# Optimization experiments

Measured on AMD Instinct MI355X. Metric: run time of the kernel, lower is better.

Reference implementation:

```python
import jax, jax.numpy as jnp
import numpy as np

LOW_DIM = 1024
PARAM_DIMS = [(1024, 768), (768,), (768, 256), (256,)]
BLOCK_DIMS = [int(np.prod(d)) for d in PARAM_DIMS]
TOTAL_DIM = int(sum(BLOCK_DIMS))          # 984064
LL = 1 << int(np.ceil(np.log2(TOTAL_DIM)))  # 1048576 = 2^20
BATCH = 32


def fwht(x):
    """Unnormalized fast Walsh-Hadamard transform over the last axis.

    x: [B, L], L a power of two. Butterfly stage order does not change the
    result (H_L = H_2^{\\otimes n}), so this matches the torch chunk/cat loop.
    """
    B, L = x.shape
    h = L // 2
    while h >= 1:
        x = x.reshape(B, -1, 2, h)
        a, b = x[:, :, 0, :], x[:, :, 1, :]
        x = jnp.stack([a + b, a - b], axis=2)
        h //= 2
    return x.reshape(B, L)


def setup_inputs() -> dict:
    key = jax.random.key(0)
    kz, kb, kg = jax.random.split(key, 3)
    z = jax.random.normal(kz, (BATCH, LOW_DIM), dtype=jnp.float32)
    # BB: random signs in {-1, +1}, as in make_fastfood_vars
    BB = jnp.where(jax.random.uniform(kb, (LL,)) < 0.5, -1.0, 1.0).astype(jnp.float32)
    GG = jax.random.normal(kg, (LL,), dtype=jnp.float32)
    Pi = jnp.asarray(np.random.default_rng(0).permutation(LL), dtype=jnp.int32)
    divisor = jnp.sqrt(LL * jnp.sum(GG ** 2)).astype(jnp.float32)
    return {"z": z, "BB": BB, "GG": GG, "divisor": divisor, "Pi": Pi}


def reference(z, BB, GG, divisor, Pi):
    # pad z from low_dim to LL
    dd = jnp.pad(z, ((0, 0), (0, LL - z.shape[1])))      # [B, LL]
    m = fwht(dd * BB[None, :])                           # H (B x)
    m = m[:, Pi] * GG[None, :]                           # G Pi H B x
    m = fwht(m)                                          # H G Pi H B x
    scale = divisor * np.float32(np.sqrt(float(TOTAL_DIM) / LL))
    delta = m[:, :TOTAL_DIM] / scale                     # [B, total_dim]
    outs = []
    off = 0
    for bd, pd in zip(BLOCK_DIMS, PARAM_DIMS):
        outs.append(delta[:, off:off + bd].reshape(-1, *pd))
        off += bd
    return tuple(outs)
```

## Files before the change

kernel.cpp:

```cpp
#include <hip/hip_runtime.h>
#include <math.h>


#define TS 17
#define TOTAL_DIM 984064
#define OUT_B0 786432
#define OUT_B1 787200
#define OUT_B2 983808
#define OFF1 25165824L
#define OFF2 25190400L
#define OFF3 31481856L

template<int CTRL>
__device__ __forceinline__ float pdpp(float x) {
    return __int_as_float(__builtin_amdgcn_update_dpp(
        0, __float_as_int(x), CTRL, 0xF, 0xF, true));
}
template<int OFS>
__device__ __forceinline__ float pswz(float x) {
    return __int_as_float(__builtin_amdgcn_ds_swizzle(__float_as_int(x), OFS));
}

__device__ __forceinline__ void fwht_wave(float v[16], int lane) {
    const float s1  = (lane & 1)  ? -1.f : 1.f;
    const float s2  = (lane & 2)  ? -1.f : 1.f;
    const float s4  = (lane & 4)  ? -1.f : 1.f;
    const float s8  = (lane & 8)  ? -1.f : 1.f;
    const float s16 = (lane & 16) ? -1.f : 1.f;
    const float s32 = (lane & 32) ? -1.f : 1.f;
    #pragma unroll
    for (int r = 0; r < 16; ++r) { float p = pdpp<0xB1>(v[r]);   v[r] = fmaf(s1,  v[r], p); }
    #pragma unroll
    for (int r = 0; r < 16; ++r) { float p = pdpp<0x4E>(v[r]);   v[r] = fmaf(s2,  v[r], p); }
    #pragma unroll
    for (int r = 0; r < 16; ++r) { float p = pswz<0x101F>(v[r]); v[r] = fmaf(s4,  v[r], p); }
    #pragma unroll
    for (int r = 0; r < 16; ++r) { float p = pswz<0x201F>(v[r]); v[r] = fmaf(s8,  v[r], p); }
    #pragma unroll
    for (int r = 0; r < 16; ++r) { float p = pswz<0x401F>(v[r]); v[r] = fmaf(s16, v[r], p); }
    #pragma unroll
    for (int r = 0; r < 16; ++r) { float p = __shfl_xor(v[r], 32, 64); v[r] = fmaf(s32, v[r], p); }
    #pragma unroll
    for (int m = 1; m <= 8; m <<= 1) {
        #pragma unroll
        for (int r = 0; r < 16; ++r) {
            if (!(r & m)) {
                float a = v[r], b = v[r | m];
                v[r] = a + b;
                v[r | m] = a - b;
            }
        }
    }
}

__global__ __launch_bounds__(1024) void k_y(const float* __restrict__ z,
                                            const float* __restrict__ BBv,
                                            float* __restrict__ y_t) {
    __shared__ float tile[1024 * TS];
    const int tid = threadIdx.x;
    const int lane = tid & 63, w = tid >> 6;
    const int b = (blockIdx.x << 4) + w;
    float v[16];
    #pragma unroll
    for (int r = 0; r < 16; ++r) {
        const int i = r * 64 + lane;
        v[r] = z[(b << 10) + i] * BBv[i];
    }
    fwht_wave(v, lane);
    #pragma unroll
    for (int r = 0; r < 16; ++r) tile[(r * 64 + lane) * TS + w] = v[r];
    __syncthreads();
    const int bcol = tid & 15, i0 = tid >> 4;
    #pragma unroll 4
    for (int s = 0; s < 16; ++s) {
        const int i = i0 + (s << 6);
        y_t[(i << 5) + (blockIdx.x << 4) + bcol] = tile[i * TS + bcol];
    }
}

__global__ __launch_bounds__(1024, 8) void k_pass1(const float* __restrict__ y_t,
                                                   const float* __restrict__ GG,
                                                   const int* __restrict__ Pi,
                                                   float* __restrict__ U) {
    __shared__ float tile[1024 * TS];
    __shared__ float g_s[1024];
    __shared__ int   p_s[1024];
    const int tid = threadIdx.x;
    const int kh = blockIdx.x, bg = blockIdx.y;
    p_s[tid] = Pi[(kh << 10) + tid] & 1023;
    g_s[tid] = GG[(kh << 10) + tid];
    __syncthreads();
    const int b = tid & 15, kl0 = tid >> 4;
    #pragma unroll 4
    for (int s = 0; s < 16; ++s) {
        const int kl = kl0 + (s << 6);
        tile[kl * TS + b] = y_t[(p_s[kl] << 5) + (bg << 4) + b] * g_s[kl];
    }
    __syncthreads();
    const int lane = tid & 63, w = tid >> 6;
    float v[16];
    #pragma unroll
    for (int r = 0; r < 16; ++r) v[r] = tile[(r * 64 + lane) * TS + w];
    fwht_wave(v, lane);
    const long ub = ((long)((bg << 4) + w) << 20) + ((long)kh << 10);
    #pragma unroll
    for (int r = 0; r < 16; ++r) U[ub + r * 64 + lane] = v[r];
}

__global__ __launch_bounds__(1024, 8) void k_pass2(const float* __restrict__ U,
                                                   const float* __restrict__ divisor,
                                                   float* __restrict__ out) {
    __shared__ float tile[1024 * TS];
    const int tid = threadIdx.x;
    const int jl0 = blockIdx.x << 4;
    const int bb  = blockIdx.y;
    const float* Ub = U + ((long)bb << 20);
    const int jl = tid & 15, k0 = tid >> 4;
    #pragma unroll 4
    for (int s = 0; s < 16; ++s) {
        const int kh = k0 + (s << 6);
        tile[kh * TS + jl] = Ub[((long)kh << 10) + jl0 + jl];
    }
    __syncthreads();
    const int lane = tid & 63, w = tid >> 6;
    float v[16];
    #pragma unroll
    for (int r = 0; r < 16; ++r) v[r] = tile[(r * 64 + lane) * TS + w];
    fwht_wave(v, lane);
    const float inv = 1.0f / (divisor[0] * sqrtf((float)TOTAL_DIM / 1048576.0f));
    #pragma unroll
    for (int r = 0; r < 16; ++r) tile[(r * 64 + lane) * TS + w] = v[r] * inv;
    __syncthreads();
    #pragma unroll 2
    for (int s = 0; s < 16; ++s) {
        const int jh = k0 + (s << 6);
        if (jh <= 960) {
            const int j = (jh << 10) + jl0 + jl;
            long oidx;
            if (j < OUT_B0)      oidx = (long)bb * 786432 + j;
            else if (j < OUT_B1) oidx = OFF1 + (long)bb * 768 + (j - OUT_B0);
            else if (j < OUT_B2) oidx = OFF2 + (long)bb * 196608 + (j - OUT_B1);
            else                 oidx = OFF3 + (long)bb * 256 + (j - OUT_B2);
            out[oidx] = tile[jh * TS + jl];
        }
    }
}

extern "C" void kernel_launch(void* const* d_in, const int* in_sizes, int n_in,
                              void* d_out, int out_size, void* d_ws, size_t ws_size,
                              hipStream_t stream) {
    const float* z   = (const float*)d_in[0];
    const float* BBv = (const float*)d_in[1];
    const float* GG  = (const float*)d_in[2];
    const float* dv  = (const float*)d_in[3];
    const int*   Pi  = (const int*)d_in[4];
    float* out = (float*)d_out;

    float* y_t = (float*)d_ws;
    float* U   = (float*)((char*)d_ws + (size_t)131072);

    k_y<<<2, 1024, 0, stream>>>(z, BBv, y_t);
    k_pass1<<<dim3(1024, 2), 1024, 0, stream>>>(y_t, GG, Pi, U);
    k_pass2<<<dim3(64, 32), 1024, 0, stream>>>(U, dv, out);
}
```

Measured before the change: 246.5 us.

## Replace cross-lane swizzle FWHT stages with LDS wave transpose and register butterflies

The 1024-point per-wave Walsh-Hadamard transform now runs a 16-point in-register butterfly, two DPP stages, then a swizzled shared-memory transpose and another 16-point in-register butterfly. This replaces the three ds_swizzle stages and the xor-32 shuffle. The transposed element ordering flows into the stores and the output tile through an XOR-swizzled shared-memory index meant to avoid bank conflicts. The cost is extra __syncthreads barriers and an LDS round trip per wave, and pass1 now writes U in a strided 4-element pattern instead of contiguous per-lane rows.

```diff
diff --git a/kernel.cpp b/kernel.cpp
--- a/kernel.cpp
+++ b/kernel.cpp
@@ -16,30 +16,8 @@
     return __int_as_float(__builtin_amdgcn_update_dpp(
         0, __float_as_int(x), CTRL, 0xF, 0xF, true));
 }
-template<int OFS>
-__device__ __forceinline__ float pswz(float x) {
-    return __int_as_float(__builtin_amdgcn_ds_swizzle(__float_as_int(x), OFS));
-}
 
-__device__ __forceinline__ void fwht_wave(float v[16], int lane) {
-    const float s1  = (lane & 1)  ? -1.f : 1.f;
-    const float s2  = (lane & 2)  ? -1.f : 1.f;
-    const float s4  = (lane & 4)  ? -1.f : 1.f;
-    const float s8  = (lane & 8)  ? -1.f : 1.f;
-    const float s16 = (lane & 16) ? -1.f : 1.f;
-    const float s32 = (lane & 32) ? -1.f : 1.f;
-    #pragma unroll
-    for (int r = 0; r < 16; ++r) { float p = pdpp<0xB1>(v[r]);   v[r] = fmaf(s1,  v[r], p); }
-    #pragma unroll
-    for (int r = 0; r < 16; ++r) { float p = pdpp<0x4E>(v[r]);   v[r] = fmaf(s2,  v[r], p); }
-    #pragma unroll
-    for (int r = 0; r < 16; ++r) { float p = pswz<0x101F>(v[r]); v[r] = fmaf(s4,  v[r], p); }
-    #pragma unroll
-    for (int r = 0; r < 16; ++r) { float p = pswz<0x201F>(v[r]); v[r] = fmaf(s8,  v[r], p); }
-    #pragma unroll
-    for (int r = 0; r < 16; ++r) { float p = pswz<0x401F>(v[r]); v[r] = fmaf(s16, v[r], p); }
-    #pragma unroll
-    for (int r = 0; r < 16; ++r) { float p = __shfl_xor(v[r], 32, 64); v[r] = fmaf(s32, v[r], p); }
+__device__ __forceinline__ void h16(float v[16]) {
     #pragma unroll
     for (int m = 1; m <= 8; m <<= 1) {
         #pragma unroll
@@ -51,6 +29,39 @@
             }
         }
     }
+}
+
+__device__ __forceinline__ void dpp2(float v[16], int lane) {
+    const float s1 = (lane & 1) ? -1.f : 1.f;
+    const float s2 = (lane & 2) ? -1.f : 1.f;
+    #pragma unroll
+    for (int r = 0; r < 16; ++r) { float p = pdpp<0xB1>(v[r]); v[r] = fmaf(s1, v[r], p); }
+    #pragma unroll
+    for (int r = 0; r < 16; ++r) { float p = pdpp<0x4E>(v[r]); v[r] = fmaf(s2, v[r], p); }
+}
+
+__device__ __forceinline__ void wave_transpose(float v[16], float* ws, int lane) {
+    #pragma unroll
+    for (int r = 0; r < 16; ++r) {
+        const int i = r * 64 + lane;
+        ws[i ^ ((r & 7) << 2)] = v[r];
+    }
+    #pragma unroll
+    for (int rp = 0; rp < 16; ++rp) {
+        const int i = (lane & 3) | (rp << 2) | ((lane >> 2) << 6);
+        v[rp] = ws[i ^ (((lane >> 2) & 7) << 2)];
+    }
+}
+
+__device__ __forceinline__ void fwht1024(float v[16], float* ws, int lane) {
+    h16(v);
+    dpp2(v, lane);
+    wave_transpose(v, ws, lane);
+    h16(v);
+}
+
+__device__ __forceinline__ int phys2(int i, int col) {
+    return (i * TS + col) ^ (((i >> 6) & 7) << 2);
 }
 
 __global__ __launch_bounds__(1024) void k_y(const float* __restrict__ z,
@@ -66,15 +77,19 @@
         const int i = r * 64 + lane;
         v[r] = z[(b << 10) + i] * BBv[i];
     }
-    fwht_wave(v, lane);
+    fwht1024(v, &tile[w << 10], lane);
+    __syncthreads();
     #pragma unroll
-    for (int r = 0; r < 16; ++r) tile[(r * 64 + lane) * TS + w] = v[r];
+    for (int rp = 0; rp < 16; ++rp) {
+        const int i = (lane & 3) | (rp << 2) | ((lane >> 2) << 6);
+        tile[phys2(i, w)] = v[rp];
+    }
     __syncthreads();
     const int bcol = tid & 15, i0 = tid >> 4;
     #pragma unroll 4
     for (int s = 0; s < 16; ++s) {
         const int i = i0 + (s << 6);
-        y_t[(i << 5) + (blockIdx.x << 4) + bcol] = tile[i * TS + bcol];
+        y_t[(i << 5) + (blockIdx.x << 4) + bcol] = tile[phys2(i, bcol)];
     }
 }
 
@@ -101,10 +116,15 @@
     float v[16];
     #pragma unroll
     for (int r = 0; r < 16; ++r) v[r] = tile[(r * 64 + lane) * TS + w];
-    fwht_wave(v, lane);
+    h16(v);
+    dpp2(v, lane);
+    __syncthreads();
+    wave_transpose(v, &tile[w << 10], lane);
+    h16(v);
     const long ub = ((long)((bg << 4) + w) << 20) + ((long)kh << 10);
+    float* Up = U + ub + (lane & 3) + ((lane >> 2) << 6);
     #pragma unroll
-    for (int r = 0; r < 16; ++r) U[ub + r * 64 + lane] = v[r];
+    for (int rp = 0; rp < 16; ++rp) Up[rp << 2] = v[rp];
 }
 
 __global__ __launch_bounds__(1024, 8) void k_pass2(const float* __restrict__ U,
@@ -114,22 +134,30 @@
     const int tid = threadIdx.x;
     const int jl0 = blockIdx.x << 4;
     const int bb  = blockIdx.y;
-    const float* Ub = U + ((long)bb << 20);
+    const float* Ubp = U + ((long)bb << 20);
     const int jl = tid & 15, k0 = tid >> 4;
     #pragma unroll 4
     for (int s = 0; s < 16; ++s) {
         const int kh = k0 + (s << 6);
-        tile[kh * TS + jl] = Ub[((long)kh << 10) + jl0 + jl];
+        tile[kh * TS + jl] = Ubp[((long)kh << 10) + jl0 + jl];
     }
     __syncthreads();
     const int lane = tid & 63, w = tid >> 6;
     float v[16];
     #pragma unroll
     for (int r = 0; r < 16; ++r) v[r] = tile[(r * 64 + lane) * TS + w];
-    fwht_wave(v, lane);
+    h16(v);
+    dpp2(v, lane);
+    __syncthreads();
+    wave_transpose(v, &tile[w << 10], lane);
+    h16(v);
     const float inv = 1.0f / (divisor[0] * sqrtf((float)TOTAL_DIM / 1048576.0f));
+    __syncthreads();
     #pragma unroll
-    for (int r = 0; r < 16; ++r) tile[(r * 64 + lane) * TS + w] = v[r] * inv;
+    for (int rp = 0; rp < 16; ++rp) {
+        const int jh = (lane & 3) | (rp << 2) | ((lane >> 2) << 6);
+        tile[phys2(jh, w)] = v[rp] * inv;
+    }
     __syncthreads();
     #pragma unroll 2
     for (int s = 0; s < 16; ++s) {
@@ -141,7 +169,7 @@
             else if (j < OUT_B1) oidx = OFF1 + (long)bb * 768 + (j - OUT_B0);
             else if (j < OUT_B2) oidx = OFF2 + (long)bb * 196608 + (j - OUT_B1);
             else                 oidx = OFF3 + (long)bb * 256 + (j - OUT_B2);
-            out[oidx] = tile[jh * TS + jl];
+            out[oidx] = tile[phys2(jh, jl)];
         }
     }
 }
```

New measurement: 258.5 us. +4.9%, slower.
